# Kernel optimization log

Measured on AMD Instinct MI355X. Metric: run time of the kernel, lower is better.

The kernel has to match this reference:

```python
import jax, jax.numpy as jnp
import numpy as np

BEAM = 8
MAX_LEN = 64
SOS_ID = 1
EOS_ID = 2
NEG = -1e30


def setup_inputs() -> dict:
    key = jax.random.key(0)
    ks = jax.random.split(key, 12)
    B, L, H, V, E = 16, 64, 1024, 32000, 1024
    s = 0.02
    return {
        "dec_hidden": jax.random.normal(ks[0], (B, H), jnp.float32),
        "q_enc_outputs": jax.random.normal(ks[1], (B, L, H), jnp.float32),
        "q_inputs_length": jax.random.randint(ks[2], (B,), 1, L + 1),
        "embedding": jax.random.normal(ks[3], (V, E), jnp.float32) * s,
        "W_ih": jax.random.normal(ks[4], (E, 3 * H), jnp.float32) * s,
        "W_hh": jax.random.normal(ks[5], (H, 3 * H), jnp.float32) * s,
        "b_ih": jnp.zeros((3 * H,), jnp.float32),
        "b_hh": jnp.zeros((3 * H,), jnp.float32),
        "W_c": jax.random.normal(ks[6], (2 * H, H), jnp.float32) * s,
        "W_out": jax.random.normal(ks[7], (H, V), jnp.float32) * s,
        "b_out": jnp.zeros((V,), jnp.float32),
    }


def _beam_search(dec_hidden, q_enc_outputs, q_inputs_length, embedding,
                 W_ih, W_hh, b_ih, b_hh, W_c, W_out, b_out):
    B, H = dec_hidden.shape
    L = q_enc_outputs.shape[1]
    V = W_out.shape[1]
    K = BEAM
    N = B * K
    pos_index = jnp.arange(B)[:, None] * K  # [B,1] offset of each batch's beam block

    # inflate encoder state beam_size times (beam is the inner dim: index = b*K + k)
    hidden = jnp.repeat(dec_hidden, K, axis=0)            # [N,H]
    q_enc = jnp.repeat(q_enc_outputs, K, axis=0)          # [N,L,H]
    q_len = jnp.repeat(q_inputs_length, K, axis=0)        # [N]
    len_mask = jnp.arange(L)[None, :] < q_len[:, None]    # [N,L]

    # only beam 0 of each batch starts live (score 0), rest -inf
    seq_scores = jnp.full((N,), NEG, jnp.float32).at[::K].set(0.0)
    dec_input = jnp.full((N,), SOS_ID, jnp.int32)

    def gru_cell(x, h):
        gx = x @ W_ih + b_ih
        gh = h @ W_hh + b_hh
        xr, xz, xn = jnp.split(gx, 3, axis=-1)
        hr, hz, hn = jnp.split(gh, 3, axis=-1)
        r = jax.nn.sigmoid(xr + hr)
        z = jax.nn.sigmoid(xz + hz)
        n = jnp.tanh(xn + r * hn)
        return (1.0 - z) * n + z * h

    def step(carry, _):
        hidden, seq_scores, dec_input = carry
        x = embedding[dec_input]                               # [N,E]
        h = gru_cell(x, hidden)                                # [N,H]
        # dot-product attention over encoder outputs
        att = jnp.einsum('nh,nlh->nl', h, q_enc) / jnp.sqrt(jnp.float32(H))
        att = jnp.where(len_mask, att, NEG)
        a = jax.nn.softmax(att, axis=-1)
        ctx = jnp.einsum('nl,nlh->nh', a, q_enc)
        o = jnp.tanh(jnp.concatenate([h, ctx], axis=-1) @ W_c)
        logits = o @ W_out + b_out                             # [N,V]
        logp = jax.nn.log_softmax(logits, axis=-1)
        # accumulate scores, flatten beams*vocab per batch, take top-K
        cand = (seq_scores[:, None] + logp).reshape(B, K * V)
        scores, idx = jax.lax.top_k(cand, K)                   # [B,K]
        symbols = (idx % V).reshape(N)
        preds = (idx // V + pos_index).reshape(N)              # predecessor beam rows
        new_hidden = h[preds]
        new_scores = scores.reshape(N)
        stored = new_scores                                     # stored before EOS mask
        new_scores = jnp.where(symbols == EOS_ID, NEG, new_scores)
        return (new_hidden, new_scores, symbols), (stored, preds, symbols)

    _, (all_scores, all_preds, all_syms) = jax.lax.scan(
        step, (hidden, seq_scores, dec_input), None, length=MAX_LEN)

    # backtrack: pick top-K final beams and trace predecessors backwards
    final_scores = all_scores[-1].reshape(B, K)
    sorted_score, sorted_idx = jax.lax.top_k(final_scores, K)
    t_pred = (sorted_idx + pos_index).reshape(N)

    def back(carry, xs):
        syms_t, preds_t = xs
        cur = syms_t[carry]
        return preds_t[carry], cur

    _, seq_rev = jax.lax.scan(back, t_pred, (all_syms[::-1], all_preds[::-1]))
    sequences = seq_rev[::-1].T.reshape(B, BEAM, MAX_LEN)
    return sorted_score, sequences


def reference(dec_hidden, q_enc_outputs, q_inputs_length, embedding,
              W_ih, W_hh, b_ih, b_hh, W_c, W_out, b_out):
    return _beam_search(dec_hidden, q_enc_outputs, q_inputs_length, embedding,
                        W_ih, W_hh, b_ih, b_hh, W_c, W_out, b_out)
```

## Files before the change

kernel.cpp:

```cpp
#include <hip/hip_runtime.h>
#include <cstdint>
#include <cstddef>
#include <climits>

#define Hdim 1024
#define Vdim 32000
#define Lq 64
#define Nrows 128
#define TMAX 64
#define NEGF (-1e30f)

__device__ __forceinline__ bool betterf(float av, int ai, float bv, int bi) {
  return (av > bv) || (av == bv && ai < bi);
}

__device__ __forceinline__ float tanh_xla(float x) {
  float ax = fabsf(x);
  float xc = fminf(fmaxf(x, -7.90531110763549805f), 7.90531110763549805f);
  float x2 = __fmul_rn(xc, xc);
  float p = -2.76076847742355e-16f;
  p = fmaf(p, x2, 2.00018790482477e-13f);
  p = fmaf(p, x2, -8.60467152213735e-11f);
  p = fmaf(p, x2, 5.12229709037114e-08f);
  p = fmaf(p, x2, 1.48572235717979e-05f);
  p = fmaf(p, x2, 6.37261928875436e-04f);
  p = fmaf(p, x2, 4.89352455891786e-03f);
  p = __fmul_rn(xc, p);
  float q = 1.19825839466702e-06f;
  q = fmaf(q, x2, 1.18534705686654e-04f);
  q = fmaf(q, x2, 2.26843463243900e-03f);
  q = fmaf(q, x2, 4.89352518554385e-03f);
  float r = __fdiv_rn(p, q);
  return (ax < 0.0004f) ? x : r;
}

__device__ __forceinline__ float sigmoid_xla(float x) {
  return __fadd_rn(0.5f, __fmul_rn(0.5f, tanh_xla(__fmul_rn(0.5f, x))));
}

__device__ __forceinline__ float exp_xla(float x) {
  x = fminf(x, 88.3762626647950f);
  x = fmaxf(x, -88.3762626647949f);
  float m = floorf(fmaf(x, 1.44269504088896341f, 0.5f));
  float r = fmaf(m, -0.693359375f, x);
  r = fmaf(m, 2.12194440e-4f, r);
  float r2 = __fmul_rn(r, r);
  float p = 1.9875691500e-4f;
  p = fmaf(p, r, 1.3981999507e-3f);
  p = fmaf(p, r, 8.3334519073e-3f);
  p = fmaf(p, r, 4.1665795894e-2f);
  p = fmaf(p, r, 1.6666665459e-1f);
  p = fmaf(p, r, 5.0000001201e-1f);
  p = fmaf(p, r2, r);
  p = __fadd_rn(p, 1.0f);
  int n = (int)m;
  float two_n = __int_as_float((n + 127) << 23);
  return __fmul_rn(p, two_n);
}

__device__ __forceinline__ float log_xla(float x) {
  int ix = __float_as_int(x);
  int e = ((ix >> 23) & 0xFF) - 126;
  float m = __int_as_float((ix & 0x007FFFFF) | 0x3F000000);
  if (m < 0.707106781186547524f) { e -= 1; m = __fadd_rn(m, m); }
  m = __fsub_rn(m, 1.0f);
  float z = __fmul_rn(m, m);
  float p = 7.0376836292e-2f;
  p = fmaf(p, m, -1.1514610310e-1f);
  p = fmaf(p, m, 1.1676998740e-1f);
  p = fmaf(p, m, -1.2420140846e-1f);
  p = fmaf(p, m, 1.4249322787e-1f);
  p = fmaf(p, m, -1.6668057665e-1f);
  p = fmaf(p, m, 2.0000714765e-1f);
  p = fmaf(p, m, -2.4999993993e-1f);
  p = fmaf(p, m, 3.3333331174e-1f);
  float ef = (float)e;
  float y = __fmul_rn(m, __fmul_rn(z, p));
  y = fmaf(ef, -2.12194440e-4f, y);
  y = fmaf(z, -0.5f, y);
  float res = __fadd_rn(m, y);
  res = fmaf(ef, 0.693359375f, res);
  return res;
}

template <int MT, int NT>
__device__ __forceinline__ void gemm_body(
    const float* __restrict__ A, int lda, const int* __restrict__ rowmap,
    const float* __restrict__ B, int ldb, const float* __restrict__ bias,
    float* __restrict__ C, int ldc, int K, int act, int n0, int m0)
{
  constexpr int RM = MT / 16, RN = NT / 16;
  constexpr int PA = MT + 4, PB = NT + 4;
  __shared__ float As[32][PA];
  __shared__ float Bs[32][PB];
  __shared__ int rows[MT];
  const int t = threadIdx.x;
  if (t < MT) rows[t] = rowmap ? rowmap[m0 + t] : (m0 + t);
  __syncthreads();
  const int tm = t >> 4, tn = t & 15;
  float acc[RM][RN] = {};
  for (int kt = 0; kt < K; kt += 32) {
#pragma unroll
    for (int i = 0; i < MT / 32; ++i) {
      int idx = t + i * 256;
      int m = idx >> 3, k4 = idx & 7;
      float4 v = *reinterpret_cast<const float4*>(
          &A[(size_t)rows[m] * lda + (size_t)(kt + k4 * 4)]);
      As[k4 * 4 + 0][m] = v.x;
      As[k4 * 4 + 1][m] = v.y;
      As[k4 * 4 + 2][m] = v.z;
      As[k4 * 4 + 3][m] = v.w;
    }
#pragma unroll
    for (int i = 0; i < NT / 32; ++i) {
      int idx = t + i * 256;
      int kk = idx / (NT / 4), n4 = idx % (NT / 4);
      float4 v = *reinterpret_cast<const float4*>(
          &B[(size_t)(kt + kk) * ldb + (size_t)(n0 + n4 * 4)]);
      *reinterpret_cast<float4*>(&Bs[kk][n4 * 4]) = v;
    }
    __syncthreads();
#pragma unroll
    for (int kk = 0; kk < 32; ++kk) {
      float a[RM], bb[RN];
      if constexpr (RM == 2) {
        float2 v = *reinterpret_cast<const float2*>(&As[kk][tm * 2]);
        a[0] = v.x; a[1] = v.y;
      } else {
#pragma unroll
        for (int c = 0; c < RM / 4; ++c) {
          float4 v = *reinterpret_cast<const float4*>(&As[kk][tm * RM + c * 4]);
          a[c * 4 + 0] = v.x; a[c * 4 + 1] = v.y;
          a[c * 4 + 2] = v.z; a[c * 4 + 3] = v.w;
        }
      }
      if constexpr (RN == 2) {
        float2 v = *reinterpret_cast<const float2*>(&Bs[kk][tn * 2]);
        bb[0] = v.x; bb[1] = v.y;
      } else {
#pragma unroll
        for (int c = 0; c < RN / 4; ++c) {
          float4 v = *reinterpret_cast<const float4*>(&Bs[kk][tn * RN + c * 4]);
          bb[c * 4 + 0] = v.x; bb[c * 4 + 1] = v.y;
          bb[c * 4 + 2] = v.z; bb[c * 4 + 3] = v.w;
        }
      }
#pragma unroll
      for (int i = 0; i < RM; ++i)
#pragma unroll
        for (int j = 0; j < RN; ++j)
          acc[i][j] = fmaf(a[i], bb[j], acc[i][j]);
    }
    __syncthreads();
  }
#pragma unroll
  for (int i = 0; i < RM; ++i) {
    int m = m0 + tm * RM + i;
#pragma unroll
    for (int j = 0; j < RN; ++j) {
      int n = n0 + tn * RN + j;
      float v = acc[i][j];
      if (bias) v = __fadd_rn(v, bias[n]);
      if (act == 1) v = tanh_xla(v);
      C[(size_t)m * ldc + n] = v;
    }
  }
}

__global__ __launch_bounds__(256) void sgemm_logits(
    const float* __restrict__ A, const float* __restrict__ B,
    const float* __restrict__ bias, float* __restrict__ C)
{
  gemm_body<128, 128>(A, 1024, nullptr, B, 32000, bias, C, 32000, 1024, 0,
                      blockIdx.x * 128, 0);
}

__global__ __launch_bounds__(256) void gates_gemm(
    const float* __restrict__ emb, const int* __restrict__ symmap,
    const float* __restrict__ W_ih,
    const float* __restrict__ hprev, const int* __restrict__ hmap,
    const float* __restrict__ W_hh,
    float* __restrict__ gA, float* __restrict__ gB)
{
  if (blockIdx.z == 0)
    gemm_body<32, 64>(emb, 1024, symmap, W_ih, 3072, nullptr, gA, 3072, 1024, 0,
                      blockIdx.x * 64, blockIdx.y * 32);
  else
    gemm_body<32, 64>(hprev, 1024, hmap, W_hh, 3072, nullptr, gB, 3072, 1024, 0,
                      blockIdx.x * 64, blockIdx.y * 32);
}

__global__ __launch_bounds__(256) void sgemm_wc(
    const float* __restrict__ A2, const float* __restrict__ W_c,
    float* __restrict__ obuf)
{
  gemm_body<32, 32>(A2, 2048, nullptr, W_c, 1024, nullptr, obuf, 1024, 2048, 1,
                    blockIdx.x * 32, blockIdx.y * 32);
}

__global__ __launch_bounds__(256) void gru_gates(
    const float* __restrict__ gA, const float* __restrict__ gB,
    const float* __restrict__ b_ih, const float* __restrict__ b_hh,
    const float* __restrict__ hprev, const int* __restrict__ hmap,
    float* __restrict__ hout, float* __restrict__ A2)
{
  int n = blockIdx.x;
  int row = hmap[n];
  const float* hp = hprev + (size_t)row * Hdim;
  const float* a = gA + (size_t)n * 3 * Hdim;
  const float* g = gB + (size_t)n * 3 * Hdim;
  for (int j = threadIdx.x; j < Hdim; j += 256) {
    float xr = __fadd_rn(a[j],            b_ih[j]);
    float xz = __fadd_rn(a[Hdim + j],     b_ih[Hdim + j]);
    float xn = __fadd_rn(a[2 * Hdim + j], b_ih[2 * Hdim + j]);
    float hr = __fadd_rn(g[j],            b_hh[j]);
    float hz = __fadd_rn(g[Hdim + j],     b_hh[Hdim + j]);
    float hn = __fadd_rn(g[2 * Hdim + j], b_hh[2 * Hdim + j]);
    float r = sigmoid_xla(__fadd_rn(xr, hr));
    float z = sigmoid_xla(__fadd_rn(xz, hz));
    float t1 = __fmul_rn(r, hn);
    float nn = tanh_xla(__fadd_rn(xn, t1));
    float u1 = __fsub_rn(1.0f, z);
    float u2 = __fmul_rn(u1, nn);
    float u3 = __fmul_rn(z, hp[j]);
    float h = __fadd_rn(u2, u3);
    hout[(size_t)n * Hdim + j] = h;
    A2[(size_t)n * 2 * Hdim + j] = h;
  }
}

__global__ __launch_bounds__(256) void attn_kernel(
    const float* __restrict__ hnew, const float* __restrict__ q_enc,
    const int* __restrict__ q_len, float* __restrict__ A2)
{
  int n = blockIdx.x;
  int b = n >> 3;
  const float* q = q_enc + (size_t)b * Lq * Hdim;
  const float* hrow = hnew + (size_t)n * Hdim;
  __shared__ float att[Lq];
  __shared__ float ebuf[Lq];
  __shared__ float s_mx, s_sum;
  int t = threadIdx.x;
  if (t < Lq) {
    const float4* h4 = reinterpret_cast<const float4*>(hrow);
    const float4* q4 = reinterpret_cast<const float4*>(q + (size_t)t * Hdim);
    float acc[8];
#pragma unroll
    for (int j = 0; j < 8; ++j) acc[j] = 0.f;
    for (int i = 0; i < 128; ++i) {
      float4 ha = h4[2 * i], hb = h4[2 * i + 1];
      float4 qa = q4[2 * i], qb = q4[2 * i + 1];
      acc[0] = fmaf(ha.x, qa.x, acc[0]);
      acc[1] = fmaf(ha.y, qa.y, acc[1]);
      acc[2] = fmaf(ha.z, qa.z, acc[2]);
      acc[3] = fmaf(ha.w, qa.w, acc[3]);
      acc[4] = fmaf(hb.x, qb.x, acc[4]);
      acc[5] = fmaf(hb.y, qb.y, acc[5]);
      acc[6] = fmaf(hb.z, qb.z, acc[6]);
      acc[7] = fmaf(hb.w, qb.w, acc[7]);
    }
    float b0 = __fadd_rn(acc[0], acc[4]);
    float b1 = __fadd_rn(acc[1], acc[5]);
    float b2 = __fadd_rn(acc[2], acc[6]);
    float b3 = __fadd_rn(acc[3], acc[7]);
    float c0 = __fadd_rn(b0, b2);
    float c1 = __fadd_rn(b1, b3);
    float dot = __fadd_rn(c0, c1);
    att[t] = __fdiv_rn(dot, 32.0f);
  }
  __syncthreads();
  if (t == 0) {
    int len = q_len[b];
    float mx = -INFINITY;
    for (int l = 0; l < Lq; ++l) {
      float v = (l < len) ? att[l] : NEGF;
      att[l] = v;
      mx = fmaxf(mx, v);
    }
    s_mx = mx;
  }
  __syncthreads();
  if (t < Lq) ebuf[t] = exp_xla(__fsub_rn(att[t], s_mx));
  __syncthreads();
  if (t == 0) {
    float acc[8];
#pragma unroll
    for (int j = 0; j < 8; ++j) acc[j] = 0.f;
    for (int i = 0; i < 8; ++i) {
#pragma unroll
      for (int j = 0; j < 8; ++j) acc[j] = __fadd_rn(acc[j], ebuf[i * 8 + j]);
    }
    float b0 = __fadd_rn(acc[0], acc[4]);
    float b1 = __fadd_rn(acc[1], acc[5]);
    float b2 = __fadd_rn(acc[2], acc[6]);
    float b3 = __fadd_rn(acc[3], acc[7]);
    float c0 = __fadd_rn(b0, b2);
    float c1 = __fadd_rn(b1, b3);
    s_sum = __fadd_rn(c0, c1);
  }
  __syncthreads();
  if (t < Lq) att[t] = __fdiv_rn(ebuf[t], s_sum);
  __syncthreads();
#pragma unroll
  for (int hh = 0; hh < 4; ++hh) {
    int h = t + hh * 256;
    float c = 0.f;
    for (int l = 0; l < Lq; ++l) c = fmaf(att[l], q[(size_t)l * Hdim + h], c);
    A2[(size_t)n * 2 * Hdim + Hdim + h] = c;
  }
}

__global__ __launch_bounds__(256) void lse_kernel(const float* __restrict__ logits,
                                                  float* __restrict__ ebuf,
                                                  float* __restrict__ mxA,
                                                  float* __restrict__ lseA)
{
  int n = blockIdx.x;
  const float* row = logits + (size_t)n * Vdim;
  float* erow = ebuf + (size_t)n * Vdim;
  int t = threadIdx.x;
  int lane = t & 63, w = t >> 6;
  const float4* row4 = reinterpret_cast<const float4*>(row);
  float4* erow4 = reinterpret_cast<float4*>(erow);
  float mx = -INFINITY;
  for (int i = t; i < 8000; i += 256) {
    float4 v = row4[i];
    mx = fmaxf(mx, fmaxf(fmaxf(v.x, v.y), fmaxf(v.z, v.w)));
  }
#pragma unroll
  for (int off = 32; off >= 1; off >>= 1) mx = fmaxf(mx, __shfl_xor(mx, off, 64));
  __shared__ float sm[4];
  __shared__ float lanes[8];
  if (lane == 0) sm[w] = mx;
  __syncthreads();
  mx = fmaxf(fmaxf(sm[0], sm[1]), fmaxf(sm[2], sm[3]));
  for (int i = t; i < 8000; i += 256) {
    float4 v = row4[i];
    float4 e;
    e.x = exp_xla(__fsub_rn(v.x, mx));
    e.y = exp_xla(__fsub_rn(v.y, mx));
    e.z = exp_xla(__fsub_rn(v.z, mx));
    e.w = exp_xla(__fsub_rn(v.w, mx));
    erow4[i] = e;
  }
  __syncthreads();
  if (t < 8) {
    float a = 0.f;
#pragma unroll 8
    for (int i = 0; i < 4000; ++i) a = __fadd_rn(a, erow[i * 8 + t]);
    lanes[t] = a;
  }
  __syncthreads();
  if (t == 0) {
    float b0 = __fadd_rn(lanes[0], lanes[4]);
    float b1 = __fadd_rn(lanes[1], lanes[5]);
    float b2 = __fadd_rn(lanes[2], lanes[6]);
    float b3 = __fadd_rn(lanes[3], lanes[7]);
    float c0 = __fadd_rn(b0, b2);
    float c1 = __fadd_rn(b1, b3);
    float s = __fadd_rn(c0, c1);
    mxA[n] = mx;
    lseA[n] = log_xla(s);
  }
}

__global__ __launch_bounds__(256) void topk_kernel(
    const float* __restrict__ logits, const float* __restrict__ mxA,
    const float* __restrict__ lseA, float* __restrict__ seq_scores,
    float* __restrict__ all_scores, int* __restrict__ all_preds,
    int* __restrict__ all_syms, int step)
{
  int b = blockIdx.x, t = threadIdx.x;
  __shared__ float s_seq[8], s_mx[8], s_lse[8];
  if (t < 8) {
    s_seq[t] = seq_scores[b * 8 + t];
    s_mx[t] = mxA[b * 8 + t];
    s_lse[t] = lseA[b * 8 + t];
  }
  __syncthreads();
  float lv[8]; int li[8];
#pragma unroll
  for (int r = 0; r < 8; ++r) { lv[r] = -INFINITY; li[r] = INT_MAX; }
  const float4* base4 = reinterpret_cast<const float4*>(logits + (size_t)b * 8 * Vdim);
  for (int c4 = t; c4 < 64000; c4 += 256) {
    float4 v4 = base4[c4];
    int cb = c4 * 4;
#pragma unroll
    for (int e = 0; e < 4; ++e) {
      int c = cb + e;
      int k = c / Vdim;
      float x = (e == 0) ? v4.x : (e == 1) ? v4.y : (e == 2) ? v4.z : v4.w;
      float sh = __fsub_rn(x, s_mx[k]);
      float lp = __fsub_rn(sh, s_lse[k]);
      float cand = __fadd_rn(s_seq[k], lp);
      if (betterf(cand, c, lv[7], li[7])) {
        lv[7] = cand; li[7] = c;
#pragma unroll
        for (int r = 7; r > 0; --r) {
          if (betterf(lv[r], li[r], lv[r - 1], li[r - 1])) {
            float tv = lv[r]; lv[r] = lv[r - 1]; lv[r - 1] = tv;
            int ti = li[r]; li[r] = li[r - 1]; li[r - 1] = ti;
          }
        }
      }
    }
  }
  __shared__ float sv[256][8];
  __shared__ int si[256][8];
#pragma unroll
  for (int r = 0; r < 8; ++r) { sv[t][r] = lv[r]; si[t][r] = li[r]; }
  __syncthreads();
  if (t == 0) {
    for (int u = 1; u < 256; ++u) {
#pragma unroll
      for (int r = 0; r < 8; ++r) {
        float v = sv[u][r]; int ix = si[u][r];
        if (betterf(v, ix, lv[7], li[7])) {
          lv[7] = v; li[7] = ix;
#pragma unroll
          for (int q = 7; q > 0; --q) {
            if (betterf(lv[q], li[q], lv[q - 1], li[q - 1])) {
              float tv = lv[q]; lv[q] = lv[q - 1]; lv[q - 1] = tv;
              int ti = li[q]; li[q] = li[q - 1]; li[q - 1] = ti;
            }
          }
        } else break;
      }
    }
#pragma unroll
    for (int r = 0; r < 8; ++r) {
      int idx = li[r];
      int sym = idx % Vdim;
      int pred = idx / Vdim + b * 8;
      int n = b * 8 + r;
      all_scores[step * Nrows + n] = lv[r];
      all_preds[step * Nrows + n] = pred;
      all_syms[step * Nrows + n] = sym;
      seq_scores[n] = (sym == 2) ? NEGF : lv[r];
    }
  }
}

__global__ void init_kernel(float* seq_scores, int* init_hmap, int* init_sym) {
  int t = threadIdx.x;
  if (t < 128) {
    seq_scores[t] = ((t & 7) == 0) ? 0.0f : NEGF;
    init_hmap[t] = t >> 3;
    init_sym[t] = 1;
  }
}

__global__ void final_topk(const float* __restrict__ all_scores,
                           int* __restrict__ tpred, float* __restrict__ out_scores) {
  int b = threadIdx.x;
  if (b >= 16) return;
  float v[8]; int ki[8];
#pragma unroll
  for (int k = 0; k < 8; ++k) { v[k] = all_scores[63 * Nrows + b * 8 + k]; ki[k] = k; }
#pragma unroll
  for (int p = 0; p < 7; ++p)
#pragma unroll
    for (int i = 0; i < 7; ++i) {
      if (!betterf(v[i], ki[i], v[i + 1], ki[i + 1])) {
        float tv = v[i]; v[i] = v[i + 1]; v[i + 1] = tv;
        int ti = ki[i]; ki[i] = ki[i + 1]; ki[i + 1] = ti;
      }
    }
#pragma unroll
  for (int j = 0; j < 8; ++j) {
    out_scores[b * 8 + j] = v[j];
    tpred[b * 8 + j] = b * 8 + ki[j];
  }
}

__global__ void backtrack(const int* __restrict__ all_syms, const int* __restrict__ all_preds,
                          const int* __restrict__ tpred, float* __restrict__ out_seq) {
  int n = threadIdx.x;
  if (n >= 128) return;
  int carry = tpred[n];
  for (int tt = 63; tt >= 0; --tt) {
    int sym = all_syms[tt * Nrows + carry];
    out_seq[(size_t)n * 64 + tt] = (float)sym;
    carry = all_preds[tt * Nrows + carry];
  }
}

extern "C" void kernel_launch(void* const* d_in, const int* in_sizes, int n_in,
                              void* d_out, int out_size, void* d_ws, size_t ws_size,
                              hipStream_t stream) {
  (void)in_sizes; (void)n_in; (void)out_size; (void)ws_size;
  const float* dec_hidden = (const float*)d_in[0];
  const float* q_enc      = (const float*)d_in[1];
  const int*   q_len      = (const int*)d_in[2];
  const float* embedding  = (const float*)d_in[3];
  const float* W_ih       = (const float*)d_in[4];
  const float* W_hh       = (const float*)d_in[5];
  const float* b_ih       = (const float*)d_in[6];
  const float* b_hh       = (const float*)d_in[7];
  const float* W_c        = (const float*)d_in[8];
  const float* W_out      = (const float*)d_in[9];
  const float* b_out      = (const float*)d_in[10];
  float* out_scores = (float*)d_out;
  float* out_seq    = (float*)d_out + 128;

  char* w = (char*)d_ws;
  auto alloc = [&](size_t bytes) {
    char* p = w;
    w += (bytes + 255) & ~(size_t)255;
    return p;
  };
  float* hbuf0 = (float*)alloc((size_t)128 * 1024 * 4);
  float* hbuf1 = (float*)alloc((size_t)128 * 1024 * 4);
  float* A2    = (float*)alloc((size_t)128 * 2048 * 4);
  float* obuf  = (float*)alloc((size_t)128 * 1024 * 4);
  float* gA    = (float*)alloc((size_t)128 * 3072 * 4);
  float* gB    = (float*)alloc((size_t)128 * 3072 * 4);
  float* logits = (float*)alloc((size_t)128 * 32000 * 4);
  float* ebuf   = (float*)alloc((size_t)128 * 32000 * 4);
  float* mxA   = (float*)alloc(128 * 4);
  float* lseA  = (float*)alloc(128 * 4);
  float* seq_scores = (float*)alloc(128 * 4);
  int* init_hmap = (int*)alloc(128 * 4);
  int* init_sym  = (int*)alloc(128 * 4);
  int* tpred     = (int*)alloc(128 * 4);
  float* all_scores = (float*)alloc((size_t)64 * 128 * 4);
  int* all_preds = (int*)alloc((size_t)64 * 128 * 4);
  int* all_syms  = (int*)alloc((size_t)64 * 128 * 4);

  init_kernel<<<1, 128, 0, stream>>>(seq_scores, init_hmap, init_sym);

  for (int t = 0; t < TMAX; ++t) {
    const int* symmap = (t == 0) ? init_sym : (all_syms + (t - 1) * Nrows);
    const int* hmap   = (t == 0) ? init_hmap : (all_preds + (t - 1) * Nrows);
    const float* hprev = (t == 0) ? dec_hidden : (((t - 1) & 1) ? hbuf1 : hbuf0);
    float* hcur = (t & 1) ? hbuf1 : hbuf0;

    gates_gemm<<<dim3(48, 4, 2), 256, 0, stream>>>(
        embedding, symmap, W_ih, hprev, hmap, W_hh, gA, gB);
    gru_gates<<<128, 256, 0, stream>>>(gA, gB, b_ih, b_hh, hprev, hmap, hcur, A2);
    attn_kernel<<<128, 256, 0, stream>>>(hcur, q_enc, q_len, A2);
    sgemm_wc<<<dim3(32, 4), 256, 0, stream>>>(A2, W_c, obuf);
    sgemm_logits<<<250, 256, 0, stream>>>(obuf, W_out, b_out, logits);
    lse_kernel<<<128, 256, 0, stream>>>(logits, ebuf, mxA, lseA);
    topk_kernel<<<16, 256, 0, stream>>>(logits, mxA, lseA, seq_scores,
                                        all_scores, all_preds, all_syms, t);
  }

  final_topk<<<1, 128, 0, stream>>>(all_scores, tpred, out_scores);
  backtrack<<<1, 128, 0, stream>>>(all_syms, all_preds, tpred, out_seq);
}
```

Baseline: 63.29 ms.

## Double-buffer GEMM tiles, swizzle B smem, retile gates GEMM, fuse GRU with attention

The shared GEMM body now uses register-staged double buffering, so the global loads for the next K tile overlap the FMA loop on the current one, with a single barrier per tile. B tiles in shared memory get an XOR column swizzle to cut bank conflicts on the float4 reads. The gates GEMM moves from 32x64 to 64x64 tiles, which halves the grid. The GRU gate kernel and the attention kernel are merged so the new hidden state stays in shared memory, removing one launch and a global reload. Shared memory per block doubles, which may lower occupancy, and the smaller gates grid offers less parallelism.

```diff
diff --git a/kernel.cpp b/kernel.cpp
--- a/kernel.cpp
+++ b/kernel.cpp
@@ -83,64 +83,93 @@
   return res;
 }
 
-template <int MT, int NT>
+__device__ __forceinline__ int bswz(int col) {
+  return col ^ (((col >> 5) & 3) << 2);
+}
+
+template <int MT, int NT, int RM, int RN>
 __device__ __forceinline__ void gemm_body(
     const float* __restrict__ A, int lda, const int* __restrict__ rowmap,
     const float* __restrict__ B, int ldb, const float* __restrict__ bias,
     float* __restrict__ C, int ldc, int K, int act, int n0, int m0)
 {
-  constexpr int RM = MT / 16, RN = NT / 16;
+  constexpr int TN = NT / RN;
   constexpr int PA = MT + 4, PB = NT + 4;
-  __shared__ float As[32][PA];
-  __shared__ float Bs[32][PB];
+  constexpr int NA = MT / 32;
+  constexpr int NB = NT / 32;
+  __shared__ float As[2][32][PA];
+  __shared__ float Bs[2][32][PB];
   __shared__ int rows[MT];
   const int t = threadIdx.x;
   if (t < MT) rows[t] = rowmap ? rowmap[m0 + t] : (m0 + t);
   __syncthreads();
-  const int tm = t >> 4, tn = t & 15;
-  float acc[RM][RN] = {};
-  for (int kt = 0; kt < K; kt += 32) {
-#pragma unroll
-    for (int i = 0; i < MT / 32; ++i) {
+  const int tm = t / TN, tn = t % TN;
+
+  float4 rA[NA], rB[NB];
+  auto load_tile = [&](int kt) {
+#pragma unroll
+    for (int i = 0; i < NA; ++i) {
       int idx = t + i * 256;
       int m = idx >> 3, k4 = idx & 7;
-      float4 v = *reinterpret_cast<const float4*>(
+      rA[i] = *reinterpret_cast<const float4*>(
           &A[(size_t)rows[m] * lda + (size_t)(kt + k4 * 4)]);
-      As[k4 * 4 + 0][m] = v.x;
-      As[k4 * 4 + 1][m] = v.y;
-      As[k4 * 4 + 2][m] = v.z;
-      As[k4 * 4 + 3][m] = v.w;
-    }
-#pragma unroll
-    for (int i = 0; i < NT / 32; ++i) {
+    }
+#pragma unroll
+    for (int i = 0; i < NB; ++i) {
       int idx = t + i * 256;
       int kk = idx / (NT / 4), n4 = idx % (NT / 4);
-      float4 v = *reinterpret_cast<const float4*>(
+      rB[i] = *reinterpret_cast<const float4*>(
           &B[(size_t)(kt + kk) * ldb + (size_t)(n0 + n4 * 4)]);
-      *reinterpret_cast<float4*>(&Bs[kk][n4 * 4]) = v;
-    }
-    __syncthreads();
+    }
+  };
+  auto store_tile = [&](int buf) {
+#pragma unroll
+    for (int i = 0; i < NA; ++i) {
+      int idx = t + i * 256;
+      int m = idx >> 3, k4 = idx & 7;
+      As[buf][k4 * 4 + 0][m] = rA[i].x;
+      As[buf][k4 * 4 + 1][m] = rA[i].y;
+      As[buf][k4 * 4 + 2][m] = rA[i].z;
+      As[buf][k4 * 4 + 3][m] = rA[i].w;
+    }
+#pragma unroll
+    for (int i = 0; i < NB; ++i) {
+      int idx = t + i * 256;
+      int kk = idx / (NT / 4), n4 = idx % (NT / 4);
+      *reinterpret_cast<float4*>(&Bs[buf][kk][bswz(n4 * 4)]) = rB[i];
+    }
+  };
+
+  float acc[RM][RN] = {};
+  load_tile(0);
+  store_tile(0);
+  __syncthreads();
+  const int ntiles = K / 32;
+  int buf = 0;
+  for (int tile = 0; tile < ntiles; ++tile) {
+    if (tile + 1 < ntiles) load_tile((tile + 1) * 32);
 #pragma unroll
     for (int kk = 0; kk < 32; ++kk) {
       float a[RM], bb[RN];
       if constexpr (RM == 2) {
-        float2 v = *reinterpret_cast<const float2*>(&As[kk][tm * 2]);
+        float2 v = *reinterpret_cast<const float2*>(&As[buf][kk][tm * 2]);
         a[0] = v.x; a[1] = v.y;
       } else {
 #pragma unroll
         for (int c = 0; c < RM / 4; ++c) {
-          float4 v = *reinterpret_cast<const float4*>(&As[kk][tm * RM + c * 4]);
+          float4 v = *reinterpret_cast<const float4*>(&As[buf][kk][tm * RM + c * 4]);
           a[c * 4 + 0] = v.x; a[c * 4 + 1] = v.y;
           a[c * 4 + 2] = v.z; a[c * 4 + 3] = v.w;
         }
       }
       if constexpr (RN == 2) {
-        float2 v = *reinterpret_cast<const float2*>(&Bs[kk][tn * 2]);
+        float2 v = *reinterpret_cast<const float2*>(&Bs[buf][kk][tn * 2]);
         bb[0] = v.x; bb[1] = v.y;
       } else {
 #pragma unroll
         for (int c = 0; c < RN / 4; ++c) {
-          float4 v = *reinterpret_cast<const float4*>(&Bs[kk][tn * RN + c * 4]);
+          float4 v = *reinterpret_cast<const float4*>(
+              &Bs[buf][kk][bswz(tn * RN + c * 4)]);
           bb[c * 4 + 0] = v.x; bb[c * 4 + 1] = v.y;
           bb[c * 4 + 2] = v.z; bb[c * 4 + 3] = v.w;
         }
@@ -151,7 +180,9 @@
         for (int j = 0; j < RN; ++j)
           acc[i][j] = fmaf(a[i], bb[j], acc[i][j]);
     }
+    if (tile + 1 < ntiles) store_tile(buf ^ 1);
     __syncthreads();
+    buf ^= 1;
   }
 #pragma unroll
   for (int i = 0; i < RM; ++i) {
@@ -171,8 +202,8 @@
     const float* __restrict__ A, const float* __restrict__ B,
     const float* __restrict__ bias, float* __restrict__ C)
 {
-  gemm_body<128, 128>(A, 1024, nullptr, B, 32000, bias, C, 32000, 1024, 0,
-                      blockIdx.x * 128, 0);
+  gemm_body<128, 128, 8, 8>(A, 1024, nullptr, B, 32000, bias, C, 32000, 1024, 0,
+                            blockIdx.x * 128, 0);
 }
 
 __global__ __launch_bounds__(256) void gates_gemm(
@@ -183,66 +214,66 @@
     float* __restrict__ gA, float* __restrict__ gB)
 {
   if (blockIdx.z == 0)
-    gemm_body<32, 64>(emb, 1024, symmap, W_ih, 3072, nullptr, gA, 3072, 1024, 0,
-                      blockIdx.x * 64, blockIdx.y * 32);
+    gemm_body<64, 64, 4, 4>(emb, 1024, symmap, W_ih, 3072, nullptr, gA, 3072,
+                            1024, 0, blockIdx.x * 64, blockIdx.y * 64);
   else
-    gemm_body<32, 64>(hprev, 1024, hmap, W_hh, 3072, nullptr, gB, 3072, 1024, 0,
-                      blockIdx.x * 64, blockIdx.y * 32);
+    gemm_body<64, 64, 4, 4>(hprev, 1024, hmap, W_hh, 3072, nullptr, gB, 3072,
+                            1024, 0, blockIdx.x * 64, blockIdx.y * 64);
 }
 
 __global__ __launch_bounds__(256) void sgemm_wc(
     const float* __restrict__ A2, const float* __restrict__ W_c,
     float* __restrict__ obuf)
 {
-  gemm_body<32, 32>(A2, 2048, nullptr, W_c, 1024, nullptr, obuf, 1024, 2048, 1,
-                    blockIdx.x * 32, blockIdx.y * 32);
-}
-
-__global__ __launch_bounds__(256) void gru_gates(
+  gemm_body<32, 32, 2, 2>(A2, 2048, nullptr, W_c, 1024, nullptr, obuf, 1024,
+                          2048, 1, blockIdx.x * 32, blockIdx.y * 32);
+}
+
+__global__ __launch_bounds__(256) void gru_attn(
     const float* __restrict__ gA, const float* __restrict__ gB,
     const float* __restrict__ b_ih, const float* __restrict__ b_hh,
     const float* __restrict__ hprev, const int* __restrict__ hmap,
+    const float* __restrict__ q_enc, const int* __restrict__ q_len,
     float* __restrict__ hout, float* __restrict__ A2)
-{
-  int n = blockIdx.x;
-  int row = hmap[n];
-  const float* hp = hprev + (size_t)row * Hdim;
-  const float* a = gA + (size_t)n * 3 * Hdim;
-  const float* g = gB + (size_t)n * 3 * Hdim;
-  for (int j = threadIdx.x; j < Hdim; j += 256) {
-    float xr = __fadd_rn(a[j],            b_ih[j]);
-    float xz = __fadd_rn(a[Hdim + j],     b_ih[Hdim + j]);
-    float xn = __fadd_rn(a[2 * Hdim + j], b_ih[2 * Hdim + j]);
-    float hr = __fadd_rn(g[j],            b_hh[j]);
-    float hz = __fadd_rn(g[Hdim + j],     b_hh[Hdim + j]);
-    float hn = __fadd_rn(g[2 * Hdim + j], b_hh[2 * Hdim + j]);
-    float r = sigmoid_xla(__fadd_rn(xr, hr));
-    float z = sigmoid_xla(__fadd_rn(xz, hz));
-    float t1 = __fmul_rn(r, hn);
-    float nn = tanh_xla(__fadd_rn(xn, t1));
-    float u1 = __fsub_rn(1.0f, z);
-    float u2 = __fmul_rn(u1, nn);
-    float u3 = __fmul_rn(z, hp[j]);
-    float h = __fadd_rn(u2, u3);
-    hout[(size_t)n * Hdim + j] = h;
-    A2[(size_t)n * 2 * Hdim + j] = h;
-  }
-}
-
-__global__ __launch_bounds__(256) void attn_kernel(
-    const float* __restrict__ hnew, const float* __restrict__ q_enc,
-    const int* __restrict__ q_len, float* __restrict__ A2)
 {
   int n = blockIdx.x;
   int b = n >> 3;
-  const float* q = q_enc + (size_t)b * Lq * Hdim;
-  const float* hrow = hnew + (size_t)n * Hdim;
+  int t = threadIdx.x;
+  __shared__ float hsh[Hdim];
   __shared__ float att[Lq];
   __shared__ float ebuf[Lq];
   __shared__ float s_mx, s_sum;
-  int t = threadIdx.x;
+
+  {
+    int row = hmap[n];
+    const float* hp = hprev + (size_t)row * Hdim;
+    const float* a = gA + (size_t)n * 3 * Hdim;
+    const float* g = gB + (size_t)n * 3 * Hdim;
+    for (int j = t; j < Hdim; j += 256) {
+      float xr = __fadd_rn(a[j],            b_ih[j]);
+      float xz = __fadd_rn(a[Hdim + j],     b_ih[Hdim + j]);
+      float xn = __fadd_rn(a[2 * Hdim + j], b_ih[2 * Hdim + j]);
+      float hr = __fadd_rn(g[j],            b_hh[j]);
+      float hz = __fadd_rn(g[Hdim + j],     b_hh[Hdim + j]);
+      float hn = __fadd_rn(g[2 * Hdim + j], b_hh[2 * Hdim + j]);
+      float r = sigmoid_xla(__fadd_rn(xr, hr));
+      float z = sigmoid_xla(__fadd_rn(xz, hz));
+      float t1 = __fmul_rn(r, hn);
+      float nn = tanh_xla(__fadd_rn(xn, t1));
+      float u1 = __fsub_rn(1.0f, z);
+      float u2 = __fmul_rn(u1, nn);
+      float u3 = __fmul_rn(z, hp[j]);
+      float h = __fadd_rn(u2, u3);
+      hout[(size_t)n * Hdim + j] = h;
+      A2[(size_t)n * 2 * Hdim + j] = h;
+      hsh[j] = h;
+    }
+  }
+  __syncthreads();
+
+  const float* q = q_enc + (size_t)b * Lq * Hdim;
   if (t < Lq) {
-    const float4* h4 = reinterpret_cast<const float4*>(hrow);
+    const float4* h4 = reinterpret_cast<const float4*>(hsh);
     const float4* q4 = reinterpret_cast<const float4*>(q + (size_t)t * Hdim);
     float acc[8];
 #pragma unroll
@@ -535,10 +566,10 @@
     const float* hprev = (t == 0) ? dec_hidden : (((t - 1) & 1) ? hbuf1 : hbuf0);
     float* hcur = (t & 1) ? hbuf1 : hbuf0;
 
-    gates_gemm<<<dim3(48, 4, 2), 256, 0, stream>>>(
+    gates_gemm<<<dim3(48, 2, 2), 256, 0, stream>>>(
         embedding, symmap, W_ih, hprev, hmap, W_hh, gA, gB);
-    gru_gates<<<128, 256, 0, stream>>>(gA, gB, b_ih, b_hh, hprev, hmap, hcur, A2);
-    attn_kernel<<<128, 256, 0, stream>>>(hcur, q_enc, q_len, A2);
+    gru_attn<<<128, 256, 0, stream>>>(gA, gB, b_ih, b_hh, hprev, hmap,
+                                      q_enc, q_len, hcur, A2);
     sgemm_wc<<<dim3(32, 4), 256, 0, stream>>>(A2, W_c, obuf);
     sgemm_logits<<<250, 256, 0, stream>>>(obuf, W_out, b_out, logits);
     lse_kernel<<<128, 256, 0, stream>>>(logits, ebuf, mxA, lseA);
```

Measured after the change: 86.45 ms. 36.6% more time.
